# Optimization experiments

Hardware: AMD Instinct MI355X
Metric: run time of the kernel (lower is better)

Reference implementation:

```python
import jax, jax.numpy as jnp
import numpy as np

B, T, C = 2, 2048, 1024
NH = 16
HD = C // NH

def setup_inputs() -> dict:
    key = jax.random.key(0)
    k1, k2, k3 = jax.random.split(key, 3)
    x = jax.random.normal(k1, (B, T, C), dtype=jnp.float32)
    w_attn = jax.random.normal(k2, (C, 3 * C), dtype=jnp.float32) * 0.02
    w_proj = jax.random.normal(k3, (C, C), dtype=jnp.float32) * 0.02
    return {"x": x, "w_attn": w_attn, "w_proj": w_proj}

def reference(x, w_attn, w_proj):
    b, t, c = x.shape
    qkv = x @ w_attn                                  # [B,T,3C]
    q, k, v = jnp.split(qkv, 3, axis=-1)
    # [B,NH,T,HD]
    q = q.reshape(b, t, NH, HD).transpose(0, 2, 1, 3)
    k = k.reshape(b, t, NH, HD).transpose(0, 2, 1, 3)
    v = v.reshape(b, t, NH, HD).transpose(0, 2, 1, 3)
    scale = 1.0 / np.sqrt(HD).astype(np.float32)
    att = jnp.einsum('bhqd,bhkd->bhqk', q, k) * scale  # [B,NH,T,T]
    causal = jnp.tril(jnp.ones((t, t), dtype=bool))
    att = jnp.where(causal[None, None], att, jnp.float32(-jnp.inf))
    att = jax.nn.softmax(att, axis=-1)
    y = jnp.einsum('bhqk,bhkd->bhqd', att, v)          # [B,NH,T,HD]
    y = y.transpose(0, 2, 1, 3).reshape(b, t, c)
    return y @ w_proj
```

## Files before the change

kernel.cpp:

```cpp
#include <hip/hip_runtime.h>
#include <hip/hip_bf16.h>

#define BB 2
#define TT 2048
#define CCH 1024
#define NHH 16
#define HDD 64
#define M_TOK (BB*TT)
#define N_QKV (3*CCH)

typedef __attribute__((ext_vector_type(8))) short bf16x8;
typedef __attribute__((ext_vector_type(4))) float f32x4;
typedef unsigned short u16;
typedef unsigned int u32;

__device__ __forceinline__ u16 f2bf(float f) {
    union { float f; u32 u; } v; v.f = f;
    u32 u = v.u;
    u32 r = (u + 0x7FFFu + ((u >> 16) & 1u)) >> 16;
    return (u16)r;
}

__device__ __forceinline__ u32 pk_bf16(float a, float b) {
    u32 ua = __float_as_uint(a) + 0x8000u;
    u32 ub = __float_as_uint(b) + 0x8000u;
    return __builtin_amdgcn_perm(ub, ua, 0x07060302u);
}

__device__ __forceinline__ void async_copy16(const void* g, void* l) {
    __builtin_amdgcn_global_load_lds((__attribute__((address_space(1))) void*)g,
                                     (__attribute__((address_space(3))) void*)l,
                                     16, 0, 0);
}


__global__ __launch_bounds__(256) void cast_bf16_kernel(
    const float* __restrict__ src, u16* __restrict__ dst, int n4) {
    int i = blockIdx.x * 256 + threadIdx.x;
    if (i < n4) {
        float4 f = ((const float4*)src)[i];
        ushort4 o;
        o.x = f2bf(f.x); o.y = f2bf(f.y); o.z = f2bf(f.z); o.w = f2bf(f.w);
        ((ushort4*)dst)[i] = o;
    }
}

__global__ __launch_bounds__(256) void transpose_bf16_kernel(
    const float* __restrict__ src, u16* __restrict__ dst, int R, int Cn,
    int scale_rows, float sc) {
    __shared__ float tile[32][33];
    int c0 = blockIdx.x * 32, r0 = blockIdx.y * 32;
    int tx = threadIdx.x, ty = threadIdx.y;
#pragma unroll
    for (int i = ty; i < 32; i += 8)
        tile[i][tx] = src[(size_t)(r0 + i) * Cn + c0 + tx];
    __syncthreads();
#pragma unroll
    for (int i = ty; i < 32; i += 8) {
        float v = tile[tx][i];
        if (c0 + i < scale_rows) v *= sc;
        dst[(size_t)(c0 + i) * R + r0 + tx] = f2bf(v);
    }
}


template<int SWAP, int NJ>
__device__ __forceinline__ void gemm_kloop(
    const u16* __restrict__ A, const u16* __restrict__ Bt, int K,
    int m0, int n0, int t, u16* __restrict__ As, u16* __restrict__ Bs,
    f32x4 (&acc)[4][4])
{
    int lane = t & 63, w = t >> 6;
    int mw = (w >> 1) * 64, nw = (w & 1) * (NJ * 16);
    int mr = lane & 15, quad = lane >> 4;

    int rA = t >> 2, ko = (t & 3) << 3;
    const u16* gA0 = A + (size_t)(m0 + rA) * K + ko;
    const u16* gA1 = A + (size_t)(m0 + 64 + rA) * K + ko;
    const u16* gB0 = Bt + (size_t)(n0 + rA) * K + ko;
    const u16* gB1 = (NJ == 4) ? Bt + (size_t)(n0 + 64 + rA) * K + ko : nullptr;
    u16* lA0 = As + (size_t)t * 8;
    u16* lA1 = As + (size_t)(256 + t) * 8;
    u16* lB0 = Bs + (size_t)t * 8;
    u16* lB1 = Bs + (size_t)(256 + t) * 8;

    for (int k0 = 0; k0 < K; k0 += 32) {
        async_copy16(gA0 + k0, lA0);
        async_copy16(gA1 + k0, lA1);
        async_copy16(gB0 + k0, lB0);
        if (NJ == 4) async_copy16(gB1 + k0, lB1);
        __syncthreads();
        bf16x8 af[4], bfr[NJ];
#pragma unroll
        for (int i = 0; i < 4; ++i)
            af[i] = *(const bf16x8*)&As[(mw + i * 16 + mr) * 32 + quad * 8];
#pragma unroll
        for (int j = 0; j < NJ; ++j)
            bfr[j] = *(const bf16x8*)&Bs[(nw + j * 16 + mr) * 32 + quad * 8];
#pragma unroll
        for (int i = 0; i < 4; ++i)
#pragma unroll
            for (int j = 0; j < NJ; ++j) {
                if (SWAP)
                    acc[i][j] = __builtin_amdgcn_mfma_f32_16x16x32_bf16(bfr[j], af[i], acc[i][j], 0, 0, 0);
                else
                    acc[i][j] = __builtin_amdgcn_mfma_f32_16x16x32_bf16(af[i], bfr[j], acc[i][j], 0, 0, 0);
            }
        __syncthreads();
    }
}


__global__ __launch_bounds__(256) void qkv_gemm_kernel(
    const u16* __restrict__ A, const u16* __restrict__ Bt,
    u16* __restrict__ Qo, u16* __restrict__ Ko, u16* __restrict__ Vto)
{
    __shared__ u16 As[128 * 32];
    __shared__ u16 Bs[128 * 32];
    int t = threadIdx.x;
    int m0 = blockIdx.y * 128, n0 = blockIdx.x * 128;
    int part = n0 >> 10;
    int lane = t & 63, w = t >> 6;
    int mw = (w >> 1) * 64, nw = (w & 1) * 64;
    int mr = lane & 15, quad = lane >> 4;

    f32x4 zero = {0.f, 0.f, 0.f, 0.f};
    f32x4 acc[4][4];
#pragma unroll
    for (int i = 0; i < 4; ++i)
#pragma unroll
        for (int j = 0; j < 4; ++j) acc[i][j] = zero;

    if (part < 2) {
        gemm_kloop<1, 4>(A, Bt, CCH, m0, n0, t, As, Bs, acc);
        u16* dstp = part ? Ko : Qo;
#pragma unroll
        for (int i = 0; i < 4; ++i)
#pragma unroll
            for (int j = 0; j < 4; ++j) {
                int tok = m0 + mw + i * 16 + mr;
                int cg0 = n0 + nw + j * 16 + quad * 4;
                int cc = cg0 & 1023;
                int h = cc >> 6, d0 = cc & 63;
                int b = tok >> 11, tt = tok & 2047;
                int bh = b * NHH + h;
                uint2 o;
                o.x = pk_bf16(acc[i][j][0], acc[i][j][1]);
                o.y = pk_bf16(acc[i][j][2], acc[i][j][3]);
                *(uint2*)&dstp[((size_t)bh * TT + tt) * HDD + d0] = o;
            }
    } else {
        gemm_kloop<0, 4>(A, Bt, CCH, m0, n0, t, As, Bs, acc);
#pragma unroll
        for (int i = 0; i < 4; ++i)
#pragma unroll
            for (int j = 0; j < 4; ++j) {
                int t0 = m0 + mw + i * 16 + quad * 4;
                int cg = n0 + nw + j * 16 + mr;
                int cc = cg & 1023;
                int h = cc >> 6, d = cc & 63;
                int b = t0 >> 11, tt0 = t0 & 2047;
                int bh = b * NHH + h;
                uint2 o;
                o.x = pk_bf16(acc[i][j][0], acc[i][j][1]);
                o.y = pk_bf16(acc[i][j][2], acc[i][j][3]);
                *(uint2*)&Vto[((size_t)bh * HDD + d) * TT + tt0] = o;
            }
    }
}


__global__ __launch_bounds__(256) void proj_gemm_kernel(
    const u16* __restrict__ A, const u16* __restrict__ Bt, float* __restrict__ Cout)
{
    __shared__ u16 As[128 * 32];
    __shared__ u16 Bs[64 * 32];
    int t = threadIdx.x;
    int m0 = blockIdx.y * 128, n0 = blockIdx.x * 64;
    int lane = t & 63, w = t >> 6;
    int mw = (w >> 1) * 64, nw = (w & 1) * 32;
    int mr = lane & 15, quad = lane >> 4;

    f32x4 zero = {0.f, 0.f, 0.f, 0.f};
    f32x4 acc[4][4];
#pragma unroll
    for (int i = 0; i < 4; ++i)
#pragma unroll
        for (int j = 0; j < 4; ++j) acc[i][j] = zero;

    gemm_kloop<1, 2>(A, Bt, CCH, m0, n0, t, As, Bs, acc);

#pragma unroll
    for (int i = 0; i < 4; ++i)
#pragma unroll
        for (int j = 0; j < 2; ++j) {
            int tok = m0 + mw + i * 16 + mr;
            int cg0 = n0 + nw + j * 16 + quad * 4;
            float4 v;
            v.x = acc[i][j][0]; v.y = acc[i][j][1];
            v.z = acc[i][j][2]; v.w = acc[i][j][3];
            *(float4*)&Cout[(size_t)tok * CCH + cg0] = v;
        }
}


#define PSTRIDE 72

template<bool MASK>
__device__ __forceinline__ void tile_compute(
    const u16* __restrict__ Ks, const u16* __restrict__ Vs, u16* __restrict__ pb,
    bf16x8 qf0, bf16x8 qf1, int m, int quad, int qcol, int kv0,
    f32x4 (&o)[4], f32x4& ls)
{
    f32x4 zero = {0.f, 0.f, 0.f, 0.f};
    int sw = m & 7;
    f32x4 st[4];
#pragma unroll
    for (int kc = 0; kc < 4; ++kc) {
        int rr = kc * 16 + m;
        bf16x8 kf0 = *(const bf16x8*)&Ks[rr * 64 + ((quad ^ sw) << 3)];
        bf16x8 kf1 = *(const bf16x8*)&Ks[rr * 64 + (((quad + 4) ^ sw) << 3)];
        f32x4 s = __builtin_amdgcn_mfma_f32_16x16x32_bf16(kf0, qf0, zero, 0, 0, 0);
        st[kc]   = __builtin_amdgcn_mfma_f32_16x16x32_bf16(kf1, qf1, s, 0, 0, 0);
    }
#pragma unroll
    for (int kc = 0; kc < 4; ++kc) {
        float e0, e1, e2, e3;
#pragma unroll
        for (int r = 0; r < 4; ++r) {
            float v = st[kc][r];
            if (MASK && (kv0 + kc * 16 + quad * 4 + r > qcol)) v = -1e30f;
            float e = __builtin_amdgcn_exp2f(v);
            ls[r] += e;
            if (r == 0) e0 = e; else if (r == 1) e1 = e; else if (r == 2) e2 = e; else e3 = e;
        }
        uint2 pk; pk.x = pk_bf16(e0, e1); pk.y = pk_bf16(e2, e3);
        *(uint2*)&pb[m * PSTRIDE + kc * 16 + quad * 4] = pk;
    }
#pragma unroll
    for (int ks = 0; ks < 2; ++ks) {
        bf16x8 pf = *(const bf16x8*)&pb[m * PSTRIDE + ks * 32 + quad * 8];
#pragma unroll
        for (int dg = 0; dg < 4; ++dg) {
            int rr = dg * 16 + m;
            bf16x8 vfr = *(const bf16x8*)&Vs[rr * 64 + (((quad + 4 * ks) ^ sw) << 3)];
            o[dg] = __builtin_amdgcn_mfma_f32_16x16x32_bf16(vfr, pf, o[dg], 0, 0, 0);
        }
    }
}

__global__ __launch_bounds__(256) void attn_kernel(
    const u16* __restrict__ Q, const u16* __restrict__ K,
    const u16* __restrict__ Vt, u16* __restrict__ Y)
{
    __shared__ u16 Ks[64 * 64];
    __shared__ u16 Vs[64 * 64];
    __shared__ u16 Pl[4][16 * PSTRIDE];
    int t = threadIdx.x;
    int w = t >> 6, lane = t & 63;
    int m = lane & 15, quad = lane >> 4;

    int bid = blockIdx.x;
    int head = bid & 31;
    int g = bid >> 5;
    int pr = (g < 8) ? g : 23 - g;
    int qbA = pr;
    int qbB = 31 - pr;
    int rowA = qbA * 64 + w * 16;
    int rowB = qbB * 64 + w * 16;

    const u16* qpA = Q + ((size_t)head * TT + rowA + m) * HDD + quad * 8;
    const u16* qpB = Q + ((size_t)head * TT + rowB + m) * HDD + quad * 8;
    bf16x8 qA0 = *(const bf16x8*)qpA;
    bf16x8 qA1 = *(const bf16x8*)(qpA + 32);
    bf16x8 qB0 = *(const bf16x8*)qpB;
    bf16x8 qB1 = *(const bf16x8*)(qpB + 32);

    const u16* kbase = K + (size_t)head * TT * HDD;
    const u16* vbase = Vt + (size_t)head * HDD * TT;
    u16* pb = &Pl[w][0];

    int lr = lane >> 3;
    int cg = (lane & 7) ^ lr;
    int r0 = w * 16 + lr, r1 = r0 + 8;
    u16* ldsK0 = Ks + (size_t)(w * 128 + lane) * 8;
    u16* ldsK1 = Ks + (size_t)(w * 128 + 64 + lane) * 8;
    u16* ldsV0 = Vs + (size_t)(w * 128 + lane) * 8;
    u16* ldsV1 = Vs + (size_t)(w * 128 + 64 + lane) * 8;

    f32x4 zero = {0.f, 0.f, 0.f, 0.f};
    f32x4 oA[4], oB[4], lsA = zero, lsB = zero;
#pragma unroll
    for (int dg = 0; dg < 4; ++dg) { oA[dg] = zero; oB[dg] = zero; }
    int qcolA = rowA + m, qcolB = rowB + m;

    for (int ic = 0; ic <= qbB; ++ic) {
        int kv0 = ic << 6;
        async_copy16(kbase + (size_t)(kv0 + r0) * 64 + cg * 8, ldsK0);
        async_copy16(kbase + (size_t)(kv0 + r1) * 64 + cg * 8, ldsK1);
        async_copy16(vbase + (size_t)r0 * TT + kv0 + cg * 8, ldsV0);
        async_copy16(vbase + (size_t)r1 * TT + kv0 + cg * 8, ldsV1);
        __syncthreads();
        if (ic < qbA)
            tile_compute<false>(Ks, Vs, pb, qA0, qA1, m, quad, qcolA, kv0, oA, lsA);
        else if (ic == qbA)
            tile_compute<true>(Ks, Vs, pb, qA0, qA1, m, quad, qcolA, kv0, oA, lsA);
        if (ic < qbB)
            tile_compute<false>(Ks, Vs, pb, qB0, qB1, m, quad, qcolB, kv0, oB, lsB);
        else
            tile_compute<true>(Ks, Vs, pb, qB0, qB1, m, quad, qcolB, kv0, oB, lsB);
        __syncthreads();
    }

    float lA = (lsA[0] + lsA[1]) + (lsA[2] + lsA[3]);
    float lB = (lsB[0] + lsB[1]) + (lsB[2] + lsB[3]);
    lA += __shfl_xor(lA, 16, 64); lA += __shfl_xor(lA, 32, 64);
    lB += __shfl_xor(lB, 16, 64); lB += __shfl_xor(lB, 32, 64);
    float invA = 1.0f / lA, invB = 1.0f / lB;

    int b = head >> 4, h = head & 15;
    size_t roA = ((size_t)(b * TT + rowA + m)) * CCH + h * HDD;
    size_t roB = ((size_t)(b * TT + rowB + m)) * CCH + h * HDD;
#pragma unroll
    for (int dg = 0; dg < 4; ++dg) {
        uint2 ov;
        ov.x = pk_bf16(oA[dg][0] * invA, oA[dg][1] * invA);
        ov.y = pk_bf16(oA[dg][2] * invA, oA[dg][3] * invA);
        *(uint2*)&Y[roA + dg * 16 + quad * 4] = ov;
        ov.x = pk_bf16(oB[dg][0] * invB, oB[dg][1] * invB);
        ov.y = pk_bf16(oB[dg][2] * invB, oB[dg][3] * invB);
        *(uint2*)&Y[roB + dg * 16 + quad * 4] = ov;
    }
}


extern "C" void kernel_launch(void* const* d_in, const int* in_sizes, int n_in,
                              void* d_out, int out_size, void* d_ws, size_t ws_size,
                              hipStream_t stream) {
    const float* x      = (const float*)d_in[0];
    const float* w_attn = (const float*)d_in[1];
    const float* w_proj = (const float*)d_in[2];
    float* out = (float*)d_out;

    char* ws = (char*)d_ws;
    u16* x_bf   = (u16*)ws; ws += (size_t)M_TOK * CCH * 2;
    u16* wqkvT  = (u16*)ws; ws += (size_t)N_QKV * CCH * 2;
    u16* wprojT = (u16*)ws; ws += (size_t)CCH * CCH * 2;
    u16* qbuf   = (u16*)ws; ws += (size_t)BB * NHH * TT * HDD * 2;
    u16* kbuf   = (u16*)ws; ws += (size_t)BB * NHH * TT * HDD * 2;
    u16* vtb    = (u16*)ws; ws += (size_t)BB * NHH * HDD * TT * 2;
    u16* yb     = (u16*)ws; ws += (size_t)M_TOK * CCH * 2;

    const float QSC = 0.125f * 1.44269504088896f;

    cast_bf16_kernel<<<dim3(M_TOK * CCH / 4 / 256), dim3(256), 0, stream>>>(x, x_bf, M_TOK * CCH / 4);
    transpose_bf16_kernel<<<dim3(N_QKV / 32, CCH / 32), dim3(32, 8), 0, stream>>>(
        w_attn, wqkvT, CCH, N_QKV, CCH, QSC);
    transpose_bf16_kernel<<<dim3(CCH / 32, CCH / 32), dim3(32, 8), 0, stream>>>(
        w_proj, wprojT, CCH, CCH, 0, 1.0f);
    qkv_gemm_kernel<<<dim3(24, 32), dim3(256), 0, stream>>>(
        x_bf, wqkvT, qbuf, kbuf, vtb);
    attn_kernel<<<dim3(512), dim3(256), 0, stream>>>(qbuf, kbuf, vtb, yb);
    proj_gemm_kernel<<<dim3(16, 32), dim3(256), 0, stream>>>(yb, wprojT, out);
}
```

Baseline: 196.7 us.

## Deepen GEMM K-tile to 64 with swizzled LDS and hoist attention K/V fragments

```diff
diff --git a/kernel.cpp b/kernel.cpp
--- a/kernel.cpp
+++ b/kernel.cpp
@@ -65,7 +65,7 @@
 
 
 template<int SWAP, int NJ>
-__device__ __forceinline__ void gemm_kloop(
+__device__ __forceinline__ void gemm_kloop64(
     const u16* __restrict__ A, const u16* __restrict__ Bt, int K,
     int m0, int n0, int t, u16* __restrict__ As, u16* __restrict__ Bs,
     f32x4 (&acc)[4][4])
@@ -73,50 +73,65 @@
     int lane = t & 63, w = t >> 6;
     int mw = (w >> 1) * 64, nw = (w & 1) * (NJ * 16);
     int mr = lane & 15, quad = lane >> 4;
-
-    int rA = t >> 2, ko = (t & 3) << 3;
-    const u16* gA0 = A + (size_t)(m0 + rA) * K + ko;
-    const u16* gA1 = A + (size_t)(m0 + 64 + rA) * K + ko;
-    const u16* gB0 = Bt + (size_t)(n0 + rA) * K + ko;
-    const u16* gB1 = (NJ == 4) ? Bt + (size_t)(n0 + 64 + rA) * K + ko : nullptr;
-    u16* lA0 = As + (size_t)t * 8;
-    u16* lA1 = As + (size_t)(256 + t) * 8;
-    u16* lB0 = Bs + (size_t)t * 8;
-    u16* lB1 = Bs + (size_t)(256 + t) * 8;
-
-    for (int k0 = 0; k0 < K; k0 += 32) {
-        async_copy16(gA0 + k0, lA0);
-        async_copy16(gA1 + k0, lA1);
-        async_copy16(gB0 + k0, lB0);
-        if (NJ == 4) async_copy16(gB1 + k0, lB1);
+    int lr = lane >> 3;
+    int cswz = (lane & 7) ^ lr;
+
+    const u16* gA[4]; u16* lA[4];
+#pragma unroll
+    for (int p = 0; p < 4; ++p) {
+        int grp = w * 4 + p;
+        gA[p] = A + (size_t)(m0 + grp * 8 + lr) * K + cswz * 8;
+        lA[p] = As + ((size_t)grp * 64 + lane) * 8;
+    }
+    const u16* gB[4]; u16* lB[4];
+#pragma unroll
+    for (int p = 0; p < NJ; ++p) {
+        int grp = w * NJ + p;
+        gB[p] = Bt + (size_t)(n0 + grp * 8 + lr) * K + cswz * 8;
+        lB[p] = Bs + ((size_t)grp * 64 + lane) * 8;
+    }
+
+    int swm = mr & 7;
+    for (int k0 = 0; k0 < K; k0 += 64) {
+#pragma unroll
+        for (int p = 0; p < 4; ++p) async_copy16(gA[p] + k0, lA[p]);
+#pragma unroll
+        for (int p = 0; p < NJ; ++p) async_copy16(gB[p] + k0, lB[p]);
         __syncthreads();
-        bf16x8 af[4], bfr[NJ];
-#pragma unroll
-        for (int i = 0; i < 4; ++i)
-            af[i] = *(const bf16x8*)&As[(mw + i * 16 + mr) * 32 + quad * 8];
-#pragma unroll
-        for (int j = 0; j < NJ; ++j)
-            bfr[j] = *(const bf16x8*)&Bs[(nw + j * 16 + mr) * 32 + quad * 8];
-#pragma unroll
-        for (int i = 0; i < 4; ++i)
+#pragma unroll
+        for (int kk = 0; kk < 2; ++kk) {
+            bf16x8 af[4], bfr[4];
+#pragma unroll
+            for (int i = 0; i < 4; ++i) {
+                int r = mw + i * 16 + mr;
+                af[i] = *(const bf16x8*)&As[r * 64 + (((kk * 4 + quad) ^ swm) << 3)];
+            }
 #pragma unroll
             for (int j = 0; j < NJ; ++j) {
-                if (SWAP)
-                    acc[i][j] = __builtin_amdgcn_mfma_f32_16x16x32_bf16(bfr[j], af[i], acc[i][j], 0, 0, 0);
-                else
-                    acc[i][j] = __builtin_amdgcn_mfma_f32_16x16x32_bf16(af[i], bfr[j], acc[i][j], 0, 0, 0);
+                int r = nw + j * 16 + mr;
+                bfr[j] = *(const bf16x8*)&Bs[r * 64 + (((kk * 4 + quad) ^ swm) << 3)];
             }
+#pragma unroll
+            for (int i = 0; i < 4; ++i)
+#pragma unroll
+                for (int j = 0; j < NJ; ++j) {
+                    if (SWAP)
+                        acc[i][j] = __builtin_amdgcn_mfma_f32_16x16x32_bf16(bfr[j], af[i], acc[i][j], 0, 0, 0);
+                    else
+                        acc[i][j] = __builtin_amdgcn_mfma_f32_16x16x32_bf16(af[i], bfr[j], acc[i][j], 0, 0, 0);
+                }
+        }
         __syncthreads();
     }
 }
 
 
-__global__ __launch_bounds__(256) void qkv_gemm_kernel(
+__global__ __launch_bounds__(256, 3) void qkv_gemm_kernel(
     const u16* __restrict__ A, const u16* __restrict__ Bt,
     u16* __restrict__ Qo, u16* __restrict__ Ko, u16* __restrict__ Vto)
 {
-    __shared__ u16 As[128 * 32];
-    __shared__ u16 Bs[128 * 32];
+    __shared__ u16 As[128 * 64];
+    __shared__ u16 Bs[128 * 64];
     int t = threadIdx.x;
     int m0 = blockIdx.y * 128, n0 = blockIdx.x * 128;
     int part = n0 >> 10;
@@ -132,7 +147,7 @@
         for (int j = 0; j < 4; ++j) acc[i][j] = zero;
 
     if (part < 2) {
-        gemm_kloop<1, 4>(A, Bt, CCH, m0, n0, t, As, Bs, acc);
+        gemm_kloop64<1, 4>(A, Bt, CCH, m0, n0, t, As, Bs, acc);
         u16* dstp = part ? Ko : Qo;
 #pragma unroll
         for (int i = 0; i < 4; ++i)
@@ -150,7 +165,7 @@
                 *(uint2*)&dstp[((size_t)bh * TT + tt) * HDD + d0] = o;
             }
     } else {
-        gemm_kloop<0, 4>(A, Bt, CCH, m0, n0, t, As, Bs, acc);
+        gemm_kloop64<0, 4>(A, Bt, CCH, m0, n0, t, As, Bs, acc);
 #pragma unroll
         for (int i = 0; i < 4; ++i)
 #pragma unroll
@@ -173,8 +188,8 @@
 __global__ __launch_bounds__(256) void proj_gemm_kernel(
     const u16* __restrict__ A, const u16* __restrict__ Bt, float* __restrict__ Cout)
 {
-    __shared__ u16 As[128 * 32];
-    __shared__ u16 Bs[64 * 32];
+    __shared__ u16 As[128 * 64];
+    __shared__ u16 Bs[64 * 64];
     int t = threadIdx.x;
     int m0 = blockIdx.y * 128, n0 = blockIdx.x * 64;
     int lane = t & 63, w = t >> 6;
@@ -188,7 +203,7 @@
 #pragma unroll
         for (int j = 0; j < 4; ++j) acc[i][j] = zero;
 
-    gemm_kloop<1, 2>(A, Bt, CCH, m0, n0, t, As, Bs, acc);
+    gemm_kloop64<1, 2>(A, Bt, CCH, m0, n0, t, As, Bs, acc);
 
 #pragma unroll
     for (int i = 0; i < 4; ++i)
@@ -208,20 +223,16 @@
 
 template<bool MASK>
 __device__ __forceinline__ void tile_compute(
-    const u16* __restrict__ Ks, const u16* __restrict__ Vs, u16* __restrict__ pb,
+    const bf16x8 (&kf)[4][2], const bf16x8 (&vf)[4][2], u16* __restrict__ pb,
     bf16x8 qf0, bf16x8 qf1, int m, int quad, int qcol, int kv0,
     f32x4 (&o)[4], f32x4& ls)
 {
     f32x4 zero = {0.f, 0.f, 0.f, 0.f};
-    int sw = m & 7;
     f32x4 st[4];
 #pragma unroll
     for (int kc = 0; kc < 4; ++kc) {
-        int rr = kc * 16 + m;
-        bf16x8 kf0 = *(const bf16x8*)&Ks[rr * 64 + ((quad ^ sw) << 3)];
-        bf16x8 kf1 = *(const bf16x8*)&Ks[rr * 64 + (((quad + 4) ^ sw) << 3)];
-        f32x4 s = __builtin_amdgcn_mfma_f32_16x16x32_bf16(kf0, qf0, zero, 0, 0, 0);
-        st[kc]   = __builtin_amdgcn_mfma_f32_16x16x32_bf16(kf1, qf1, s, 0, 0, 0);
+        f32x4 s = __builtin_amdgcn_mfma_f32_16x16x32_bf16(kf[kc][0], qf0, zero, 0, 0, 0);
+        st[kc]   = __builtin_amdgcn_mfma_f32_16x16x32_bf16(kf[kc][1], qf1, s, 0, 0, 0);
     }
 #pragma unroll
     for (int kc = 0; kc < 4; ++kc) {
@@ -241,11 +252,8 @@
     for (int ks = 0; ks < 2; ++ks) {
         bf16x8 pf = *(const bf16x8*)&pb[m * PSTRIDE + ks * 32 + quad * 8];
 #pragma unroll
-        for (int dg = 0; dg < 4; ++dg) {
-            int rr = dg * 16 + m;
-            bf16x8 vfr = *(const bf16x8*)&Vs[rr * 64 + (((quad + 4 * ks) ^ sw) << 3)];
-            o[dg] = __builtin_amdgcn_mfma_f32_16x16x32_bf16(vfr, pf, o[dg], 0, 0, 0);
-        }
+        for (int dg = 0; dg < 4; ++dg)
+            o[dg] = __builtin_amdgcn_mfma_f32_16x16x32_bf16(vf[dg][ks], pf, o[dg], 0, 0, 0);
     }
 }
 
@@ -293,6 +301,7 @@
 #pragma unroll
     for (int dg = 0; dg < 4; ++dg) { oA[dg] = zero; oB[dg] = zero; }
     int qcolA = rowA + m, qcolB = rowB + m;
+    int sw = m & 7;
 
     for (int ic = 0; ic <= qbB; ++ic) {
         int kv0 = ic << 6;
@@ -301,14 +310,23 @@
         async_copy16(vbase + (size_t)r0 * TT + kv0 + cg * 8, ldsV0);
         async_copy16(vbase + (size_t)r1 * TT + kv0 + cg * 8, ldsV1);
         __syncthreads();
+        bf16x8 kf[4][2], vf[4][2];
+#pragma unroll
+        for (int kc = 0; kc < 4; ++kc) {
+            int rr = kc * 16 + m;
+            kf[kc][0] = *(const bf16x8*)&Ks[rr * 64 + ((quad ^ sw) << 3)];
+            kf[kc][1] = *(const bf16x8*)&Ks[rr * 64 + (((quad + 4) ^ sw) << 3)];
+            vf[kc][0] = *(const bf16x8*)&Vs[rr * 64 + ((quad ^ sw) << 3)];
+            vf[kc][1] = *(const bf16x8*)&Vs[rr * 64 + (((quad + 4) ^ sw) << 3)];
+        }
         if (ic < qbA)
-            tile_compute<false>(Ks, Vs, pb, qA0, qA1, m, quad, qcolA, kv0, oA, lsA);
+            tile_compute<false>(kf, vf, pb, qA0, qA1, m, quad, qcolA, kv0, oA, lsA);
         else if (ic == qbA)
-            tile_compute<true>(Ks, Vs, pb, qA0, qA1, m, quad, qcolA, kv0, oA, lsA);
+            tile_compute<true>(kf, vf, pb, qA0, qA1, m, quad, qcolA, kv0, oA, lsA);
         if (ic < qbB)
-            tile_compute<false>(Ks, Vs, pb, qB0, qB1, m, quad, qcolB, kv0, oB, lsB);
+            tile_compute<false>(kf, vf, pb, qB0, qB1, m, quad, qcolB, kv0, oB, lsB);
         else
-            tile_compute<true>(Ks, Vs, pb, qB0, qB1, m, quad, qcolB, kv0, oB, lsB);
+            tile_compute<true>(kf, vf, pb, qB0, qB1, m, quad, qcolB, kv0, oB, lsB);
         __syncthreads();
     }
 
```

After: 177.8 us. -9.6%, faster.
